# Optimization experiments

Measured on AMD Instinct MI355X. Metric: run time of the kernel, lower is better.

Reference implementation:

```python
import jax, jax.numpy as jnp
import numpy as np

D_MODEL = 1024
NUM_HEADS = 16
NEG_INF = jnp.float32(-(2.0 ** 32) + 1.0)  # matches TF's -2**32+1 padding value


def setup_inputs() -> dict:
    key = jax.random.key(0)
    ks = jax.random.split(key, 10)
    B, S, D = 4, 1024, D_MODEL
    s = 1.0 / np.sqrt(D)
    return {
        "q": jax.random.normal(ks[0], (B, S, D), jnp.float32),
        "k": jax.random.normal(ks[1], (B, S, D), jnp.float32),
        "v": jax.random.normal(ks[2], (B, S, D), jnp.float32),
        "mask": jax.random.randint(ks[3], (NUM_HEADS * B, 1, S), 0, 2, jnp.int32),
        "Wq": jax.random.normal(ks[4], (D, D), jnp.float32) * s,
        "bq": jnp.zeros((D,), jnp.float32),
        "Wk": jax.random.normal(ks[5], (D, D), jnp.float32) * s,
        "bk": jnp.zeros((D,), jnp.float32),
        "Wv": jax.random.normal(ks[6], (D, D), jnp.float32) * s,
        "bv": jnp.zeros((D,), jnp.float32),
    }


def _split_heads(x, h):
    # TF: concat(split(x, h, axis=2), axis=0) -> head index leading on batch dim
    B, S, D = x.shape
    dh = D // h
    return x.reshape(B, S, h, dh).transpose(2, 0, 1, 3).reshape(h * B, S, dh)


def _merge_heads(x, h):
    hB, S, dh = x.shape
    B = hB // h
    return x.reshape(h, B, S, dh).transpose(1, 2, 0, 3).reshape(B, S, h * dh)


def reference(q, k, v, mask, Wq, bq, Wk, bk, Wv, bv):
    h = NUM_HEADS
    qp = q @ Wq + bq
    kp = k @ Wk + bk
    vp = v @ Wv + bv
    qh = _split_heads(qp, h)  # [h*B, S, dh]
    kh = _split_heads(kp, h)
    vh = _split_heads(vp, h)
    dh = kh.shape[-1]
    logits = jnp.einsum('bqd,bkd->bqk', qh, kh) / jnp.sqrt(jnp.float32(dh))
    logits = jnp.where(mask == 0, NEG_INF, logits)  # padding mask, broadcast [h*B,1,S]
    S = qh.shape[1]
    causal = jnp.tril(jnp.ones((S, S), jnp.bool_))
    logits = jnp.where(causal[None], logits, NEG_INF)
    attn = jax.nn.softmax(logits, axis=-1)
    out = jnp.einsum('bqk,bkd->bqd', attn, vh)
    return _merge_heads(out, h)  # [B, S, d_model]
```

## Files before the change

kernel.cpp:

```cpp
#include <hip/hip_runtime.h>
#include <stdint.h>

#define DEV __device__ __forceinline__

typedef __attribute__((ext_vector_type(4))) float f32x4;
typedef __attribute__((ext_vector_type(8))) __bf16 bf16x8;
typedef __attribute__((ext_vector_type(8))) unsigned short ushort8;

DEV unsigned short f2bf(float f) {
    union { float f; unsigned int u; } v; v.f = f;
    unsigned int r = v.u + 0x7FFFu + ((v.u >> 16) & 1u);
    return (unsigned short)(r >> 16);
}
DEV float bf2f(unsigned short u) {
    union { unsigned int u; float f; } v; v.u = ((unsigned int)u) << 16;
    return v.f;
}
DEV int swz(int o) { return o ^ ((o >> 3) & 0x70); }

DEV void gload_lds16(const void* gptr, void* lptr) {
    __builtin_amdgcn_global_load_lds(
        (const __attribute__((address_space(1))) unsigned int*)gptr,
        (__attribute__((address_space(3))) unsigned int*)lptr, 16, 0, 0);
}

__global__ void k_convert(const float* __restrict__ q, const float* __restrict__ k,
                          const float* __restrict__ v, unsigned short* __restrict__ qb,
                          unsigned short* __restrict__ kb, unsigned short* __restrict__ vb) {
    const int z = blockIdx.z;
    const float* src = z == 0 ? q : (z == 1 ? k : v);
    unsigned short* dst = z == 0 ? qb : (z == 1 ? kb : vb);
    const size_t idx = ((size_t)blockIdx.x * 256 + threadIdx.x) * 8;
    f32x4 a = *(const f32x4*)(src + idx);
    f32x4 b = *(const f32x4*)(src + idx + 4);
    ushort8 o;
    o[0] = f2bf(a[0]); o[1] = f2bf(a[1]); o[2] = f2bf(a[2]); o[3] = f2bf(a[3]);
    o[4] = f2bf(b[0]); o[5] = f2bf(b[1]); o[6] = f2bf(b[2]); o[7] = f2bf(b[3]);
    *(ushort8*)(dst + idx) = o;
}

__global__ void k_convw(const float* __restrict__ Wq, const float* __restrict__ Wk,
                        const float* __restrict__ Wv, unsigned short* __restrict__ wt) {
    __shared__ float tile[64 * 65];
    const int z = blockIdx.z;
    const float* W = z == 0 ? Wq : (z == 1 ? Wk : Wv);
    unsigned short* dst = wt + (size_t)z * 1048576;
    const int k0 = blockIdx.x * 64, n0 = blockIdx.y * 64;
    const int t = threadIdx.x;
#pragma unroll
    for (int i = 0; i < 4; i++) {
        const int idx = i * 256 + t;
        const int row = idx >> 4, c4 = (idx & 15) * 4;
        f32x4 val = *(const f32x4*)(W + (size_t)(k0 + row) * 1024 + n0 + c4);
#pragma unroll
        for (int j = 0; j < 4; j++) tile[row * 65 + c4 + j] = val[j];
    }
    __syncthreads();
#pragma unroll
    for (int i = 0; i < 2; i++) {
        const int idx = i * 256 + t;
        const int nrow = idx >> 3, c8 = (idx & 7) * 8;
        ushort8 o;
#pragma unroll
        for (int j = 0; j < 8; j++) o[j] = f2bf(tile[(c8 + j) * 65 + nrow]);
        *(ushort8*)(dst + (size_t)(n0 + nrow) * 1024 + k0 + c8) = o;
    }
}

__global__ __launch_bounds__(256) void k_proj(
    const unsigned short* __restrict__ qb, const unsigned short* __restrict__ kb,
    const unsigned short* __restrict__ vb, const unsigned short* __restrict__ wt,
    const float* __restrict__ bq, const float* __restrict__ bk, const float* __restrict__ bv,
    unsigned short* __restrict__ qh, unsigned short* __restrict__ kh,
    unsigned short* __restrict__ vh) {
    const int z = blockIdx.z;
    const unsigned short* A  = z == 0 ? qb : (z == 1 ? kb : vb);
    const unsigned short* Bt = wt + (size_t)z * 1048576;
    const float* bias = z == 0 ? bq : (z == 1 ? bk : bv);
    unsigned short* outp = z == 0 ? qh : (z == 1 ? kh : vh);
    const float scale = z == 0 ? 0.125f : 1.0f;

    __shared__ unsigned short sA[128 * 64];
    __shared__ unsigned short sB[128 * 64];

    const int tid = threadIdx.x;
    const int w = tid >> 6, lane = tid & 63;
    const int c = lane & 15, gq = lane >> 4;
    const int wrow = w >> 1, wcol = w & 1;
    const int m0 = blockIdx.y * 128, n0 = blockIdx.x * 128;
    const int lr = lane >> 3;
    const int lcs = ((lane & 7) ^ (lane >> 3)) * 8;

    f32x4 acc[4][4] = {};

    for (int kt = 0; kt < 16; kt++) {
        __syncthreads();
        const int kb0 = kt * 64;
#pragma unroll
        for (int i = 0; i < 4; i++) {
            const int rbase = w * 32 + i * 8;
            gload_lds16(A  + (size_t)(m0 + rbase + lr) * 1024 + kb0 + lcs,
                        (char*)sA + rbase * 128);
            gload_lds16(Bt + (size_t)(n0 + rbase + lr) * 1024 + kb0 + lcs,
                        (char*)sB + rbase * 128);
        }
        __syncthreads();
#pragma unroll
        for (int kk = 0; kk < 2; kk++) {
            bf16x8 af[4], bfr[4];
#pragma unroll
            for (int i = 0; i < 4; i++) {
                af[i]  = *(const bf16x8*)((char*)sA +
                          swz((wrow * 64 + i * 16 + c) * 128 + kk * 64 + gq * 16));
                bfr[i] = *(const bf16x8*)((char*)sB +
                          swz((wcol * 64 + i * 16 + c) * 128 + kk * 64 + gq * 16));
            }
#pragma unroll
            for (int mi = 0; mi < 4; mi++)
#pragma unroll
                for (int ni = 0; ni < 4; ni++)
                    acc[mi][ni] = __builtin_amdgcn_mfma_f32_16x16x32_bf16(
                        af[mi], bfr[ni], acc[mi][ni], 0, 0, 0);
        }
    }

    float bvals[4];
#pragma unroll
    for (int ni = 0; ni < 4; ni++) bvals[ni] = bias[n0 + wcol * 64 + ni * 16 + c];

#pragma unroll
    for (int mi = 0; mi < 4; mi++)
#pragma unroll
        for (int ni = 0; ni < 4; ni++) {
            const int n = n0 + wcol * 64 + ni * 16 + c;
            const int head = n >> 6, d = n & 63;
#pragma unroll
            for (int r = 0; r < 4; r++) {
                const int m = m0 + wrow * 64 + mi * 16 + gq * 4 + r;
                const int bb = m >> 10, s = m & 1023;
                const float val = (acc[mi][ni][r] + bvals[ni]) * scale;
                outp[(size_t)((head << 2) + bb) * 65536 + (size_t)s * 64 + d] = f2bf(val);
            }
        }
}

__global__ void k_trv(const unsigned short* __restrict__ vh, unsigned short* __restrict__ vt) {
    __shared__ unsigned int tile[64 * 65];
    const int hb = blockIdx.y, s0 = blockIdx.x * 64;
    const int t = threadIdx.x;
#pragma unroll
    for (int it = 0; it < 2; it++) {
        const int idx = it * 256 + t;
        const int row = idx >> 3, c8 = (idx & 7) * 8;
        ushort8 val = *(const ushort8*)(vh + (size_t)hb * 65536 + (size_t)(s0 + row) * 64 + c8);
#pragma unroll
        for (int j = 0; j < 8; j++) tile[row * 65 + c8 + j] = val[j];
    }
    __syncthreads();
#pragma unroll
    for (int it = 0; it < 2; it++) {
        const int idx = it * 256 + t;
        const int d = idx >> 3, s8 = (idx & 7) * 8;
        ushort8 o;
#pragma unroll
        for (int j = 0; j < 8; j++) o[j] = (unsigned short)tile[(s8 + j) * 65 + d];
        *(ushort8*)(vt + (size_t)hb * 65536 + (size_t)d * 1024 + s0 + s8) = o;
    }
}

__global__ void k_vmean(const unsigned short* __restrict__ vh, float* __restrict__ vmean) {
    __shared__ float red[256];
    const int hb = blockIdx.x, t = threadIdx.x;
    const int d = t & 63, part = t >> 6;
    float sum = 0.f;
    const unsigned short* p = vh + (size_t)hb * 65536 + (size_t)part * 256 * 64 + d;
    for (int s = 0; s < 256; s++) sum += bf2f(p[s * 64]);
    red[t] = sum;
    __syncthreads();
    if (part == 0)
        vmean[hb * 64 + d] = (red[d] + red[64 + d] + red[128 + d] + red[192 + d]) * (1.0f / 1024.0f);
}

__global__ __launch_bounds__(256) void k_attn(
    const unsigned short* __restrict__ qh, const unsigned short* __restrict__ kh,
    const unsigned short* __restrict__ vt, const int* __restrict__ mask,
    const float* __restrict__ vmean, float* __restrict__ out) {
    __shared__ unsigned short sK[64 * 64];
    __shared__ unsigned short sV[64 * 64];
    __shared__ unsigned short sP[4 * 16 * 64];

    const int qt = blockIdx.x, hb = blockIdx.y;
    const int tid = threadIdx.x;
    const int w = tid >> 6, lane = tid & 63;
    const int c = lane & 15, g = lane >> 4;
    const int q0 = qt * 64 + w * 16;
    const int bidx = hb & 3, head = hb >> 2;

    bf16x8 aq[2];
#pragma unroll
    for (int kk = 0; kk < 2; kk++)
        aq[kk] = *(const bf16x8*)(qh + (size_t)hb * 65536 + (size_t)(q0 + c) * 64 + kk * 32 + g * 8);

    f32x4 oacc[4] = {};
    float lsum[4] = {0.f, 0.f, 0.f, 0.f};
    float mrow[4] = {-1e30f, -1e30f, -1e30f, -1e30f};
    const int* mp = mask + hb * 1024;
    unsigned short* pw = sP + w * 1024;

    for (int t = 0; t <= qt; t++) {
        const int kv0 = t * 64;
        __syncthreads();
        if (w < 2) {
            const int tl = w * 64 + lane;
#pragma unroll
            for (int i = 0; i < 4; i++) {
                const int idx = i * 128 + tl;
                const int row = idx >> 3, c8 = (idx & 7) * 8;
                bf16x8 val = *(const bf16x8*)(kh + (size_t)hb * 65536 +
                                              (size_t)(kv0 + row) * 64 + c8);
                *(bf16x8*)((char*)sK + swz(row * 128 + c8 * 2)) = val;
            }
        } else {
            const int tl = (w - 2) * 64 + lane;
#pragma unroll
            for (int i = 0; i < 4; i++) {
                const int idx = i * 128 + tl;
                const int d = idx >> 3, s8 = (idx & 7) * 8;
                bf16x8 val = *(const bf16x8*)(vt + (size_t)hb * 65536 +
                                              (size_t)d * 1024 + kv0 + s8);
                *(bf16x8*)((char*)sV + swz(d * 128 + s8 * 2)) = val;
            }
        }
        __syncthreads();

        f32x4 sacc[4] = {};
#pragma unroll
        for (int ns = 0; ns < 4; ns++) {
            const int kvl = ns * 16 + c;
#pragma unroll
            for (int kk = 0; kk < 2; kk++) {
                bf16x8 bk = *(const bf16x8*)((char*)sK + swz(kvl * 128 + kk * 64 + g * 16));
                sacc[ns] = __builtin_amdgcn_mfma_f32_16x16x32_bf16(aq[kk], bk, sacc[ns], 0, 0, 0);
            }
        }

        float sv[4][4];
#pragma unroll
        for (int ns = 0; ns < 4; ns++) {
            const int kvg = kv0 + ns * 16 + c;
            const int mv = mp[kvg];
#pragma unroll
            for (int r = 0; r < 4; r++) {
                const int qg = q0 + g * 4 + r;
                sv[ns][r] = (mv != 0 && kvg <= qg) ? sacc[ns][r] : -1e30f;
            }
        }
#pragma unroll
        for (int r = 0; r < 4; r++) {
            float vmax = fmaxf(fmaxf(sv[0][r], sv[1][r]), fmaxf(sv[2][r], sv[3][r]));
            vmax = fmaxf(vmax, __shfl_xor(vmax, 1, 64));
            vmax = fmaxf(vmax, __shfl_xor(vmax, 2, 64));
            vmax = fmaxf(vmax, __shfl_xor(vmax, 4, 64));
            vmax = fmaxf(vmax, __shfl_xor(vmax, 8, 64));
            const float mnew = fmaxf(mrow[r], vmax);
            const float alpha = __expf(mrow[r] - mnew);
            mrow[r] = mnew;
            float rs = 0.f;
            const int ql = g * 4 + r;
#pragma unroll
            for (int ns = 0; ns < 4; ns++) {
                const float pv = __expf(sv[ns][r] - mnew);
                rs += pv;
                *(unsigned short*)((char*)pw + swz(ql * 128 + (ns * 16 + c) * 2)) = f2bf(pv);
            }
            rs += __shfl_xor(rs, 1, 64);
            rs += __shfl_xor(rs, 2, 64);
            rs += __shfl_xor(rs, 4, 64);
            rs += __shfl_xor(rs, 8, 64);
            lsum[r] = lsum[r] * alpha + rs;
#pragma unroll
            for (int nd = 0; nd < 4; nd++) oacc[nd][r] *= alpha;
        }

        asm volatile("s_waitcnt lgkmcnt(0)" ::: "memory");
#pragma unroll
        for (int ks = 0; ks < 2; ks++) {
            const bf16x8 ap = *(const bf16x8*)((char*)pw + swz(c * 128 + ks * 64 + g * 16));
#pragma unroll
            for (int nd = 0; nd < 4; nd++) {
                const int d = nd * 16 + c;
                const bf16x8 bv = *(const bf16x8*)((char*)sV + swz(d * 128 + ks * 64 + g * 16));
                oacc[nd] = __builtin_amdgcn_mfma_f32_16x16x32_bf16(ap, bv, oacc[nd], 0, 0, 0);
            }
        }
    }

#pragma unroll
    for (int nd = 0; nd < 4; nd++)
#pragma unroll
        for (int r = 0; r < 4; r++) {
            const int s = q0 + g * 4 + r;
            const int dcol = nd * 16 + c;
            const float val = (mrow[r] < -5e29f) ? vmean[hb * 64 + dcol]
                                                 : oacc[nd][r] / lsum[r];
            out[(size_t)bidx * 1048576 + (size_t)s * 1024 + head * 64 + dcol] = val;
        }
}

extern "C" void kernel_launch(void* const* d_in, const int* in_sizes, int n_in,
                              void* d_out, int out_size, void* d_ws, size_t ws_size,
                              hipStream_t stream) {
    const float* q  = (const float*)d_in[0];
    const float* k  = (const float*)d_in[1];
    const float* v  = (const float*)d_in[2];
    const int* mask = (const int*)d_in[3];
    const float* Wq = (const float*)d_in[4];
    const float* bq = (const float*)d_in[5];
    const float* Wk = (const float*)d_in[6];
    const float* bk = (const float*)d_in[7];
    const float* Wv = (const float*)d_in[8];
    const float* bv = (const float*)d_in[9];
    float* out = (float*)d_out;

    unsigned short* qb = (unsigned short*)d_ws;
    unsigned short* kb = qb + 4194304;
    unsigned short* vb = kb + 4194304;
    unsigned short* wt = vb + 4194304;
    unsigned short* qh = wt + 3 * 1048576;
    unsigned short* kh = qh + 4194304;
    unsigned short* vh = kh + 4194304;
    unsigned short* vt = vh + 4194304;
    float* vmean = (float*)(vt + 4194304);

    k_convert<<<dim3(2048, 1, 3), 256, 0, stream>>>(q, k, v, qb, kb, vb);
    k_convw<<<dim3(16, 16, 3), 256, 0, stream>>>(Wq, Wk, Wv, wt);
    k_proj<<<dim3(8, 32, 3), 256, 0, stream>>>(qb, kb, vb, wt, bq, bk, bv, qh, kh, vh);
    k_trv<<<dim3(16, 64), 256, 0, stream>>>(vh, vt);
    k_vmean<<<64, 256, 0, stream>>>(vh, vmean);
    k_attn<<<dim3(16, 64), 256, 0, stream>>>(qh, kh, vt, mask, vmean, out);
}
```

Measured before the change: 243.7 us.

## Pair causal query tiles per block and double-buffer K/V via async LDS loads

Each attention block now handles two query tiles (b and 15-b) so causal work per block is balanced, halving the grid. K/V tiles are staged into double-buffered LDS with global_load_lds so the next tile's loads overlap compute on the current one. vmean now reads the transposed V with vectorized loads. LDS use doubles and there are fewer blocks, which may lower occupancy and parallelism on a large GPU.

```diff
diff --git a/kernel.cpp b/kernel.cpp
--- a/kernel.cpp
+++ b/kernel.cpp
@@ -168,82 +168,87 @@
     }
 }
 
-__global__ void k_vmean(const unsigned short* __restrict__ vh, float* __restrict__ vmean) {
+__global__ void k_vmean(const unsigned short* __restrict__ vt, float* __restrict__ vmean) {
     __shared__ float red[256];
     const int hb = blockIdx.x, t = threadIdx.x;
-    const int d = t & 63, part = t >> 6;
+    const int d = t >> 2, part = t & 3;
+    const unsigned short* p = vt + (size_t)hb * 65536 + (size_t)d * 1024 + part * 256;
     float sum = 0.f;
-    const unsigned short* p = vh + (size_t)hb * 65536 + (size_t)part * 256 * 64 + d;
-    for (int s = 0; s < 256; s++) sum += bf2f(p[s * 64]);
+#pragma unroll 4
+    for (int i = 0; i < 32; i++) {
+        ushort8 v8 = *(const ushort8*)(p + i * 8);
+#pragma unroll
+        for (int j = 0; j < 8; j++) sum += bf2f(v8[j]);
+    }
     red[t] = sum;
     __syncthreads();
     if (part == 0)
-        vmean[hb * 64 + d] = (red[d] + red[64 + d] + red[128 + d] + red[192 + d]) * (1.0f / 1024.0f);
+        vmean[hb * 64 + d] = (red[t] + red[t + 1] + red[t + 2] + red[t + 3]) * (1.0f / 1024.0f);
 }
 
 __global__ __launch_bounds__(256) void k_attn(
     const unsigned short* __restrict__ qh, const unsigned short* __restrict__ kh,
     const unsigned short* __restrict__ vt, const int* __restrict__ mask,
     const float* __restrict__ vmean, float* __restrict__ out) {
-    __shared__ unsigned short sK[64 * 64];
-    __shared__ unsigned short sV[64 * 64];
-    __shared__ unsigned short sP[4 * 16 * 64];
-
-    const int qt = blockIdx.x, hb = blockIdx.y;
+    __shared__ unsigned short sK[2][64 * 64];
+    __shared__ unsigned short sV[2][64 * 64];
+    __shared__ unsigned short sP[2][4 * 16 * 64];
+
+    const int b = blockIdx.x, hb = blockIdx.y;
     const int tid = threadIdx.x;
     const int w = tid >> 6, lane = tid & 63;
     const int c = lane & 15, g = lane >> 4;
-    const int q0 = qt * 64 + w * 16;
+    const int qtA = b, qtB = 15 - b;
+    const int tmax = qtB;
+    const int q0A = qtA * 64 + w * 16, q0B = qtB * 64 + w * 16;
     const int bidx = hb & 3, head = hb >> 2;
-
-    bf16x8 aq[2];
-#pragma unroll
-    for (int kk = 0; kk < 2; kk++)
-        aq[kk] = *(const bf16x8*)(qh + (size_t)hb * 65536 + (size_t)(q0 + c) * 64 + kk * 32 + g * 8);
-
-    f32x4 oacc[4] = {};
-    float lsum[4] = {0.f, 0.f, 0.f, 0.f};
-    float mrow[4] = {-1e30f, -1e30f, -1e30f, -1e30f};
+    const size_t hboff = (size_t)hb * 65536;
     const int* mp = mask + hb * 1024;
-    unsigned short* pw = sP + w * 1024;
-
-    for (int t = 0; t <= qt; t++) {
+
+    bf16x8 aqA[2], aqB[2];
+#pragma unroll
+    for (int kk = 0; kk < 2; kk++) {
+        aqA[kk] = *(const bf16x8*)(qh + hboff + (size_t)(q0A + c) * 64 + kk * 32 + g * 8);
+        aqB[kk] = *(const bf16x8*)(qh + hboff + (size_t)(q0B + c) * 64 + kk * 32 + g * 8);
+    }
+
+    f32x4 oaccA[4] = {}, oaccB[4] = {};
+    float lsumA[4] = {0.f, 0.f, 0.f, 0.f}, lsumB[4] = {0.f, 0.f, 0.f, 0.f};
+    float mrowA[4] = {-1e30f, -1e30f, -1e30f, -1e30f};
+    float mrowB[4] = {-1e30f, -1e30f, -1e30f, -1e30f};
+
+    const int srow = tid >> 3, sch = tid & 7;
+    const int ssc = (sch ^ (srow & 7)) * 8;
+
+    auto stage = [&](int t, int buf) {
         const int kv0 = t * 64;
-        __syncthreads();
-        if (w < 2) {
-            const int tl = w * 64 + lane;
-#pragma unroll
-            for (int i = 0; i < 4; i++) {
-                const int idx = i * 128 + tl;
-                const int row = idx >> 3, c8 = (idx & 7) * 8;
-                bf16x8 val = *(const bf16x8*)(kh + (size_t)hb * 65536 +
-                                              (size_t)(kv0 + row) * 64 + c8);
-                *(bf16x8*)((char*)sK + swz(row * 128 + c8 * 2)) = val;
-            }
-        } else {
-            const int tl = (w - 2) * 64 + lane;
-#pragma unroll
-            for (int i = 0; i < 4; i++) {
-                const int idx = i * 128 + tl;
-                const int d = idx >> 3, s8 = (idx & 7) * 8;
-                bf16x8 val = *(const bf16x8*)(vt + (size_t)hb * 65536 +
-                                              (size_t)d * 1024 + kv0 + s8);
-                *(bf16x8*)((char*)sV + swz(d * 128 + s8 * 2)) = val;
-            }
-        }
-        __syncthreads();
-
+#pragma unroll
+        for (int i = 0; i < 2; i++) {
+            const int row = i * 32 + srow;
+            gload_lds16(kh + hboff + (size_t)(kv0 + row) * 64 + ssc,
+                        (char*)sK[buf] + row * 128 + sch * 16);
+        }
+#pragma unroll
+        for (int i = 0; i < 2; i++) {
+            const int row = i * 32 + srow;
+            gload_lds16(vt + hboff + (size_t)row * 1024 + kv0 + ssc,
+                        (char*)sV[buf] + row * 128 + sch * 16);
+        }
+    };
+
+    auto compute_tile = [&](int kv0, int q0, const bf16x8* aq, f32x4* oacc,
+                            float* lsum, float* mrow, unsigned short* pw,
+                            const unsigned short* sKc, const unsigned short* sVc) {
         f32x4 sacc[4] = {};
 #pragma unroll
         for (int ns = 0; ns < 4; ns++) {
             const int kvl = ns * 16 + c;
 #pragma unroll
             for (int kk = 0; kk < 2; kk++) {
-                bf16x8 bk = *(const bf16x8*)((char*)sK + swz(kvl * 128 + kk * 64 + g * 16));
+                bf16x8 bk = *(const bf16x8*)((char*)sKc + swz(kvl * 128 + kk * 64 + g * 16));
                 sacc[ns] = __builtin_amdgcn_mfma_f32_16x16x32_bf16(aq[kk], bk, sacc[ns], 0, 0, 0);
             }
         }
-
         float sv[4][4];
 #pragma unroll
         for (int ns = 0; ns < 4; ns++) {
@@ -281,7 +286,6 @@
 #pragma unroll
             for (int nd = 0; nd < 4; nd++) oacc[nd][r] *= alpha;
         }
-
         asm volatile("s_waitcnt lgkmcnt(0)" ::: "memory");
 #pragma unroll
         for (int ks = 0; ks < 2; ks++) {
@@ -289,22 +293,48 @@
 #pragma unroll
             for (int nd = 0; nd < 4; nd++) {
                 const int d = nd * 16 + c;
-                const bf16x8 bv = *(const bf16x8*)((char*)sV + swz(d * 128 + ks * 64 + g * 16));
+                const bf16x8 bv = *(const bf16x8*)((char*)sVc + swz(d * 128 + ks * 64 + g * 16));
                 oacc[nd] = __builtin_amdgcn_mfma_f32_16x16x32_bf16(ap, bv, oacc[nd], 0, 0, 0);
             }
         }
-    }
-
-#pragma unroll
-    for (int nd = 0; nd < 4; nd++)
-#pragma unroll
-        for (int r = 0; r < 4; r++) {
-            const int s = q0 + g * 4 + r;
-            const int dcol = nd * 16 + c;
-            const float val = (mrow[r] < -5e29f) ? vmean[hb * 64 + dcol]
-                                                 : oacc[nd][r] / lsum[r];
-            out[(size_t)bidx * 1048576 + (size_t)s * 1024 + head * 64 + dcol] = val;
-        }
+    };
+
+    stage(0, 0);
+    for (int t = 0; t <= tmax; t++) {
+        const int cur = t & 1;
+        if (t < tmax) {
+            stage(t + 1, cur ^ 1);
+            asm volatile("s_waitcnt vmcnt(4)" ::: "memory");
+        } else {
+            asm volatile("s_waitcnt vmcnt(0)" ::: "memory");
+        }
+        __builtin_amdgcn_s_barrier();
+        __builtin_amdgcn_sched_barrier(0);
+        const int kv0 = t * 64;
+        if (t <= qtA)
+            compute_tile(kv0, q0A, aqA, oaccA, lsumA, mrowA,
+                         sP[0] + w * 1024, sK[cur], sV[cur]);
+        compute_tile(kv0, q0B, aqB, oaccB, lsumB, mrowB,
+                     sP[1] + w * 1024, sK[cur], sV[cur]);
+        __builtin_amdgcn_sched_barrier(0);
+        __builtin_amdgcn_s_barrier();
+        __builtin_amdgcn_sched_barrier(0);
+    }
+
+    auto write_out = [&](int q0, f32x4* oacc, float* lsum, float* mrow) {
+#pragma unroll
+        for (int nd = 0; nd < 4; nd++)
+#pragma unroll
+            for (int r = 0; r < 4; r++) {
+                const int s = q0 + g * 4 + r;
+                const int dcol = nd * 16 + c;
+                const float val = (mrow[r] < -5e29f) ? vmean[hb * 64 + dcol]
+                                                     : oacc[nd][r] / lsum[r];
+                out[(size_t)bidx * 1048576 + (size_t)s * 1024 + head * 64 + dcol] = val;
+            }
+    };
+    write_out(q0A, oaccA, lsumA, mrowA);
+    write_out(q0B, oaccB, lsumB, mrowB);
 }
 
 extern "C" void kernel_launch(void* const* d_in, const int* in_sizes, int n_in,
@@ -336,6 +366,6 @@
     k_convw<<<dim3(16, 16, 3), 256, 0, stream>>>(Wq, Wk, Wv, wt);
     k_proj<<<dim3(8, 32, 3), 256, 0, stream>>>(qb, kb, vb, wt, bq, bk, bv, qh, kh, vh);
     k_trv<<<dim3(16, 64), 256, 0, stream>>>(vh, vt);
-    k_vmean<<<64, 256, 0, stream>>>(vh, vmean);
-    k_attn<<<dim3(16, 64), 256, 0, stream>>>(qh, kh, vt, mask, vmean, out);
-}
+    k_vmean<<<64, 256, 0, stream>>>(vt, vmean);
+    k_attn<<<dim3(8, 64), 256, 0, stream>>>(qh, kh, vt, mask, vmean, out);
+}
```

Result: faster. 220.9 us (-9.4%).
